# Kernel optimization log

Measured on AMD Instinct MI355X. Metric: run time of the kernel, lower is better.

The kernel has to match this reference:

```python
import jax, jax.numpy as jnp
import numpy as np
from jax import lax

D_MODEL, D_STATE, D_CONV, EXPAND = 192, 16, 3, 2
D_INNER = EXPAND * D_MODEL          # 384
DT_RANK = -(-D_MODEL // 16)         # 12
LN_EPS = 1e-5


def setup_inputs() -> dict:
    key = jax.random.key(0)
    ks = jax.random.split(key, 12)
    B, H, W = 4, 64, 64
    inv_sq = lambda n: 1.0 / np.sqrt(n)
    x = jax.random.normal(ks[0], (B, H, W, D_MODEL), jnp.float32)
    prompt = jax.random.normal(ks[1], (B, H, W, D_MODEL), jnp.float32)
    W_in = jax.random.normal(ks[2], (D_MODEL, 2 * D_INNER), jnp.float32) * inv_sq(D_MODEL)
    conv_w = jax.random.normal(ks[3], (D_INNER, 1, D_CONV, D_CONV), jnp.float32) * inv_sq(D_CONV * D_CONV)
    conv_b = jax.random.normal(ks[4], (D_INNER,), jnp.float32) * 0.02
    Wx = jax.random.normal(ks[5], (D_INNER, DT_RANK + 2 * D_STATE), jnp.float32) * inv_sq(D_INNER)
    Wdt = jax.random.uniform(ks[6], (DT_RANK, D_INNER), jnp.float32, -DT_RANK ** -0.5, DT_RANK ** -0.5)
    # dt bias init: inverse softplus of dt ~ LogUniform(1e-3, 0.1)
    dt = jnp.exp(jax.random.uniform(ks[7], (D_INNER,), jnp.float32) * (np.log(0.1) - np.log(1e-3)) + np.log(1e-3))
    dt = jnp.clip(dt, 1e-4, None)
    b_dt = dt + jnp.log(-jnp.expm1(-dt))
    A_log = jnp.log(jnp.broadcast_to(jnp.arange(1, D_STATE + 1, dtype=jnp.float32), (D_INNER, D_STATE)))
    D = jnp.ones((D_INNER,), jnp.float32)
    Wp = jax.random.normal(ks[8], (D_MODEL, D_STATE), jnp.float32) * inv_sq(D_MODEL)
    ln_g = jnp.ones((D_INNER,), jnp.float32)
    ln_b = jnp.zeros((D_INNER,), jnp.float32)
    Wout = jax.random.normal(ks[9], (D_INNER, D_MODEL), jnp.float32) * inv_sq(D_INNER)
    return dict(x=x, prompt=prompt, W_in=W_in, conv_w=conv_w, conv_b=conv_b, Wx=Wx,
                Wdt=Wdt, b_dt=b_dt, A_log=A_log, D=D, Wp=Wp, ln_g=ln_g, ln_b=ln_b, Wout=Wout)


def _selective_scan(u, delta, A, Bs, Cs, D):
    # u, delta: [B, L, d]; Bs, Cs: [B, L, n]; A: [d, n]; D: [d]
    Bsz = u.shape[0]
    h0 = jnp.zeros((Bsz, D_INNER, D_STATE), u.dtype)

    def step(h, inp):
        dl, uu, b, c = inp                      # [B,d],[B,d],[B,n],[B,n]
        dA = jnp.exp(dl[..., None] * A)          # [B,d,n]
        h = dA * h + (dl * uu)[..., None] * b[:, None, :]
        y = jnp.einsum('bdn,bn->bd', h, c)
        return h, y

    xs = (jnp.moveaxis(delta, 1, 0), jnp.moveaxis(u, 1, 0),
          jnp.moveaxis(Bs, 1, 0), jnp.moveaxis(Cs, 1, 0))
    _, ys = lax.scan(step, h0, xs)               # ys: [L,B,d]
    return jnp.moveaxis(ys, 0, 1) + u * D        # [B,L,d]


def reference(x, prompt, W_in, conv_w, conv_b, Wx, Wdt, b_dt, A_log, D, Wp, ln_g, ln_b, Wout):
    B, H, W, C = x.shape
    L = H * W
    xz = x @ W_in                                 # [B,H,W,2*d_inner]
    xi, z = jnp.split(xz, 2, axis=-1)
    # depthwise conv2d (NCHW, groups=d_inner)
    xc = jnp.transpose(xi, (0, 3, 1, 2))
    pad = (D_CONV - 1) // 2
    xc = lax.conv_general_dilated(xc, conv_w, (1, 1), [(pad, pad), (pad, pad)],
                                  dimension_numbers=('NCHW', 'OIHW', 'NCHW'),
                                  feature_group_count=D_INNER)
    xc = xc + conv_b[None, :, None, None]
    xc = jax.nn.silu(xc)
    u = jnp.transpose(xc.reshape(B, D_INNER, L), (0, 2, 1))   # [B,L,d]
    x_dbl = u @ Wx                                            # [B,L,r+2n]
    dtr = x_dbl[..., :DT_RANK]
    Bs = x_dbl[..., DT_RANK:DT_RANK + D_STATE]
    Cs = x_dbl[..., DT_RANK + D_STATE:]
    delta = jax.nn.softplus(dtr @ Wdt + b_dt)                 # [B,L,d] (delta_bias + softplus)
    Cs = Cs + prompt.reshape(B, L, C) @ Wp                    # prompt-conditioned C
    A = -jnp.exp(A_log)                                       # [d,n]
    y = _selective_scan(u, delta, A, Bs, Cs, D)               # [B,L,d]
    # out_norm (LayerNorm over d_inner)
    mu = jnp.mean(y, axis=-1, keepdims=True)
    var = jnp.mean(jnp.square(y - mu), axis=-1, keepdims=True)
    y = (y - mu) * lax.rsqrt(var + LN_EPS) * ln_g + ln_b
    y = y.reshape(B, H, W, D_INNER)
    y = y * jax.nn.silu(z)
    return y @ Wout
```

## Files before the change

### kernel.cpp

```cpp
#include <hip/hip_runtime.h>
#include <hip/hip_bf16.h>

#define BB 4
#define HH 64
#define WW 64
#define LL 4096
#define DM 192
#define DI 384
#define NS 16
#define RK 12
#define NC 256
#define CH 16
#define ROWS 16384
#define XDS 64
#define LOG2E 1.44269504f

typedef __bf16 bf16x8 __attribute__((ext_vector_type(8)));
typedef float  f32x4  __attribute__((ext_vector_type(4)));

#if defined(__has_builtin)
#if __has_builtin(__builtin_amdgcn_exp2f)
#define fexp2(x) __builtin_amdgcn_exp2f(x)
#else
#define fexp2(x) exp2f(x)
#endif
#else
#define fexp2(x) exp2f(x)
#endif

__device__ __forceinline__ float fsilu(float x) {
    return x / (1.0f + __expf(-x));
}

__device__ __forceinline__ unsigned short f2bf(float f) {
    unsigned int u = __float_as_uint(f);
    unsigned int r = (u + 0x7fffu + ((u >> 16) & 1u)) >> 16;
    return (unsigned short)r;
}

__global__ __launch_bounds__(256) void f32_to_bf16_vec(
    const float* __restrict__ src, unsigned short* __restrict__ dst, int n4)
{
    int i = blockIdx.x * 256 + threadIdx.x;
    if (i < n4) {
        float4 v = ((const float4*)src)[i];
        ((ushort4*)dst)[i] = make_ushort4(f2bf(v.x), f2bf(v.y), f2bf(v.z), f2bf(v.w));
    }
}

__global__ __launch_bounds__(256) void build_bt(
    const float* __restrict__ src, unsigned short* __restrict__ dst,
    int K, int Nsrc, int Nrows)
{
    int idx = blockIdx.x * 256 + threadIdx.x;
    if (idx >= Nrows * K) return;
    int n = idx / K, k = idx % K;
    dst[idx] = (n < Nsrc) ? f2bf(src[k * Nsrc + n]) : (unsigned short)0;
}

template<bool SPLIT>
__global__ __launch_bounds__(256) void gemm_bf16_mfma(
    const unsigned short* __restrict__ A, const unsigned short* __restrict__ BT,
    float* __restrict__ C0, float* __restrict__ C1,
    int M, int N, int K, int halfN)
{
    __shared__ __align__(16) char lds[64 * 80 * 2];
    char* As = lds;
    char* Bs = lds + 64 * 80;
    const int tid = threadIdx.x;
    const int w = tid >> 6, lane = tid & 63;
    const int wm = w >> 1, wn = w & 1;
    const int row0 = blockIdx.x * 64, col0 = blockIdx.y * 64;
    const int r = tid >> 2, cch = tid & 3;
    const int l15 = lane & 15, k8 = lane >> 4;

    f32x4 acc[2][2] = {};
    for (int k0 = 0; k0 < K; k0 += 32) {
        *(float4*)(As + r * 80 + cch * 16) =
            *(const float4*)(A + (size_t)(row0 + r) * K + k0 + cch * 8);
        *(float4*)(Bs + r * 80 + cch * 16) =
            *(const float4*)(BT + (size_t)(col0 + r) * K + k0 + cch * 8);
        __syncthreads();
        bf16x8 a0 = *(const bf16x8*)(As + (wm * 32 +      l15) * 80 + k8 * 16);
        bf16x8 a1 = *(const bf16x8*)(As + (wm * 32 + 16 + l15) * 80 + k8 * 16);
        bf16x8 b0 = *(const bf16x8*)(Bs + (wn * 32 +      l15) * 80 + k8 * 16);
        bf16x8 b1 = *(const bf16x8*)(Bs + (wn * 32 + 16 + l15) * 80 + k8 * 16);
        acc[0][0] = __builtin_amdgcn_mfma_f32_16x16x32_bf16(a0, b0, acc[0][0], 0, 0, 0);
        acc[0][1] = __builtin_amdgcn_mfma_f32_16x16x32_bf16(a0, b1, acc[0][1], 0, 0, 0);
        acc[1][0] = __builtin_amdgcn_mfma_f32_16x16x32_bf16(a1, b0, acc[1][0], 0, 0, 0);
        acc[1][1] = __builtin_amdgcn_mfma_f32_16x16x32_bf16(a1, b1, acc[1][1], 0, 0, 0);
        __syncthreads();
    }

    float* Cw;
    int cbase, cstride;
    if (SPLIT) {
        cstride = halfN;
        if (col0 < halfN) { Cw = C0; cbase = col0; }
        else              { Cw = C1; cbase = col0 - halfN; }
    } else {
        Cw = C0; cbase = col0; cstride = N;
    }
    #pragma unroll
    for (int fm = 0; fm < 2; ++fm)
        #pragma unroll
        for (int fn = 0; fn < 2; ++fn)
            #pragma unroll
            for (int reg = 0; reg < 4; ++reg) {
                int row = row0 + wm * 32 + fm * 16 + k8 * 4 + reg;
                int col = cbase + wn * 32 + fn * 16 + l15;
                Cw[(size_t)row * cstride + col] = acc[fm][fn][reg];
            }
}

__global__ __launch_bounds__(256) void conv_dw_silu(
    const float* __restrict__ xi, const float* __restrict__ conv_w,
    const float* __restrict__ conv_b, float* __restrict__ u,
    unsigned short* __restrict__ u_bf)
{
    int idx = blockIdx.x * 256 + threadIdx.x;
    int c4 = idx % 96;
    int rest = idx / 96;
    int w = rest % WW; rest /= WW;
    int h = rest % HH;
    int b = rest / HH;
    int c = c4 * 4;

    float wgt[4][9];
    #pragma unroll
    for (int q = 0; q < 4; ++q)
        #pragma unroll
        for (int t = 0; t < 9; ++t)
            wgt[q][t] = conv_w[(c + q) * 9 + t];

    float4 acc = *(const float4*)&conv_b[c];
    #pragma unroll
    for (int kh = 0; kh < 3; ++kh) {
        int hh = h + kh - 1;
        if ((unsigned)hh >= HH) continue;
        #pragma unroll
        for (int kw = 0; kw < 3; ++kw) {
            int ww = w + kw - 1;
            if ((unsigned)ww >= WW) continue;
            const float4 xv = *(const float4*)&xi[(((size_t)(b * HH + hh)) * WW + ww) * DI + c];
            int t = kh * 3 + kw;
            acc.x += xv.x * wgt[0][t];
            acc.y += xv.y * wgt[1][t];
            acc.z += xv.z * wgt[2][t];
            acc.w += xv.w * wgt[3][t];
        }
    }
    acc.x = fsilu(acc.x); acc.y = fsilu(acc.y);
    acc.z = fsilu(acc.z); acc.w = fsilu(acc.w);
    size_t off = (((size_t)b * LL) + h * WW + w) * DI + c;
    *(float4*)&u[off] = acc;
    *(ushort4*)&u_bf[off] = make_ushort4(f2bf(acc.x), f2bf(acc.y), f2bf(acc.z), f2bf(acc.w));
}

__global__ __launch_bounds__(256) void post_proj(
    const float* __restrict__ xdbl, const float* __restrict__ prompt,
    const float* __restrict__ Wdt, const float* __restrict__ b_dt,
    const float* __restrict__ Wp,
    float* __restrict__ delta, float* __restrict__ Csv)
{
    const int wid = threadIdx.x >> 6, lane = threadIdx.x & 63;
    const int row = blockIdx.x * 4 + wid;

    const float4* dp = (const float4*)&xdbl[(size_t)row * XDS];
    const float4 d0 = dp[0], d1 = dp[1], d2 = dp[2];
    const float dtr[RK] = {d0.x, d0.y, d0.z, d0.w, d1.x, d1.y, d1.z, d1.w,
                           d2.x, d2.y, d2.z, d2.w};

    const int n16 = lane & 15, g = lane >> 4;
    const float* prow = prompt + (size_t)row * DM + g * 48;
    float pw = 0.f;
    #pragma unroll
    for (int cc = 0; cc < 48; cc += 4) {
        const float4 p4 = *(const float4*)&prow[cc];
        const int c = g * 48 + cc;
        pw += p4.x * Wp[(c    ) * NS + n16];
        pw += p4.y * Wp[(c + 1) * NS + n16];
        pw += p4.z * Wp[(c + 2) * NS + n16];
        pw += p4.w * Wp[(c + 3) * NS + n16];
    }
    pw += __shfl_xor(pw, 16);
    pw += __shfl_xor(pw, 32);
    if (lane < 16)
        Csv[(size_t)row * NS + lane] = xdbl[(size_t)row * XDS + 28 + lane] + pw;

    #pragma unroll
    for (int jj = 0; jj < 6; ++jj) {
        int dch = jj * 64 + lane;
        float acc = b_dt[dch];
        #pragma unroll
        for (int r = 0; r < RK; ++r) acc += dtr[r] * Wdt[r * DI + dch];
        delta[(size_t)row * DI + dch] = (acc > 20.f) ? acc : log1pf(__expf(acc));
    }
}

__global__ __launch_bounds__(256) void scan_p1_v4(
    const float* __restrict__ delta, const float* __restrict__ u,
    const float* __restrict__ xdbl, const float* __restrict__ A_log,
    float* __restrict__ AH)
{
    const int g = blockIdx.x * 256 + threadIdx.x;
    const int d = g % DI;
    const int bc = g / DI;
    const int b = bc / NC, c = bc % NC;

    float Adn[NS], h[NS];
    {
        const float4* ap4 = (const float4*)(A_log + d * NS);
        #pragma unroll
        for (int q = 0; q < 4; ++q) {
            const float4 v = ap4[q];
            Adn[q*4+0] = -__expf(v.x) * LOG2E;
            Adn[q*4+1] = -__expf(v.y) * LOG2E;
            Adn[q*4+2] = -__expf(v.z) * LOG2E;
            Adn[q*4+3] = -__expf(v.w) * LOG2E;
        }
    }
    #pragma unroll
    for (int n = 0; n < NS; ++n) h[n] = 0.f;

    const size_t rbase = (size_t)(b * LL + c * CH);
    const float* dp = delta + rbase * DI + d;
    const float* up = u     + rbase * DI + d;
    const float* xp = xdbl  + rbase * XDS + 12;

    float dlt = dp[0], uu = up[0];
    float4 bb0 = *(const float4*)(xp + 0), bb1 = *(const float4*)(xp + 4);
    float4 bb2 = *(const float4*)(xp + 8), bb3 = *(const float4*)(xp + 12);
    float sdlt = 0.f;

    for (int i = 0; i < CH; ++i) {
        const float dlt_n = dp[(i + 1) * DI];
        const float uu_n  = up[(i + 1) * DI];
        const float* xn = xp + (i + 1) * XDS;
        const float4 bn0 = *(const float4*)(xn + 0), bn1 = *(const float4*)(xn + 4);
        const float4 bn2 = *(const float4*)(xn + 8), bn3 = *(const float4*)(xn + 12);

        const float du = dlt * uu;
        sdlt += dlt;
        const float bs[NS] = {bb0.x, bb0.y, bb0.z, bb0.w, bb1.x, bb1.y, bb1.z, bb1.w,
                              bb2.x, bb2.y, bb2.z, bb2.w, bb3.x, bb3.y, bb3.z, bb3.w};
        #pragma unroll
        for (int n = 0; n < NS; ++n) {
            const float a = fexp2(dlt * Adn[n]);
            h[n] = a * h[n] + du * bs[n];
        }
        dlt = dlt_n; uu = uu_n;
        bb0 = bn0; bb1 = bn1; bb2 = bn2; bb3 = bn3;
    }
    float* dst = AH + 2 * (((size_t)bc * DI + d) * NS);
    #pragma unroll
    for (int q = 0; q < 8; ++q) {
        const float ap0 = fexp2(sdlt * Adn[2*q]);
        const float ap1 = fexp2(sdlt * Adn[2*q+1]);
        *(float4*)(dst + 4 * q) = make_float4(ap0, h[2*q], ap1, h[2*q+1]);
    }
}

__global__ __launch_bounds__(256) void scan_p2(float2* __restrict__ AH)
{
    const int gid = blockIdx.x * 256 + threadIdx.x;
    const int dn = gid % (DI * NS);
    const int b  = gid / (DI * NS);
    const size_t base = (size_t)b * NC * DI * NS + dn;
    const size_t cs = (size_t)DI * NS;

    float2 buf[4];
    #pragma unroll
    for (int k = 0; k < 4; ++k) buf[k] = AH[base + (size_t)k * cs];

    float hin = 0.f;
    for (int c = 0; c < NC; c += 4) {
        #pragma unroll
        for (int k = 0; k < 4; ++k) {
            const int cn = (c + k + 4 < NC) ? (c + k + 4) : (NC - 1);
            const float2 nxt = AH[base + (size_t)cn * cs];
            const float2 cur = buf[k];
            AH[base + (size_t)(c + k) * cs].x = hin;
            hin = cur.x * hin + cur.y;
            buf[k] = nxt;
        }
    }
}

__global__ __launch_bounds__(384) void scan_p3_ln(
    const float* __restrict__ delta, const float* __restrict__ u,
    const float* __restrict__ xdbl, const float* __restrict__ Csv,
    const float* __restrict__ AH, const float* __restrict__ A_log,
    const float* __restrict__ Dvec, const float* __restrict__ z,
    const float* __restrict__ ln_g, const float* __restrict__ ln_b,
    unsigned short* __restrict__ yin_bf)
{
    __shared__ float red_s[2][8], red_sq[2][8];
    const int d = threadIdx.x;
    const int bc = blockIdx.x;
    const int b = bc / NC, c = bc % NC;
    const int wid = d >> 6, lane = d & 63;

    float Adn[NS], h[NS];
    {
        const float4* ap4 = (const float4*)(A_log + d * NS);
        #pragma unroll
        for (int q = 0; q < 4; ++q) {
            const float4 v = ap4[q];
            Adn[q*4+0] = -__expf(v.x) * LOG2E;
            Adn[q*4+1] = -__expf(v.y) * LOG2E;
            Adn[q*4+2] = -__expf(v.z) * LOG2E;
            Adn[q*4+3] = -__expf(v.w) * LOG2E;
        }
    }
    {
        const float* hp = AH + 2 * (((size_t)bc * DI + d) * NS);
        #pragma unroll
        for (int q = 0; q < 8; ++q) {
            const float4 v = *(const float4*)(hp + 4 * q);
            h[2*q] = v.x; h[2*q+1] = v.z;
        }
    }
    const float Dd = Dvec[d];
    const float lg = ln_g[d], lb = ln_b[d];

    const size_t rbase = (size_t)(b * LL + c * CH);
    const float* dp = delta + rbase * DI + d;
    const float* up = u     + rbase * DI + d;
    const float* zp = z     + rbase * DI + d;
    const float* xp = xdbl  + rbase * XDS + 12;
    const float* cp = Csv   + rbase * NS;
    unsigned short* yp = yin_bf + rbase * DI + d;

    float dlt = dp[0], uu = up[0], zz = zp[0];
    float4 bb0 = *(const float4*)(xp + 0), bb1 = *(const float4*)(xp + 4);
    float4 bb2 = *(const float4*)(xp + 8), bb3 = *(const float4*)(xp + 12);
    float4 cc0 = *(const float4*)(cp + 0), cc1 = *(const float4*)(cp + 4);
    float4 cc2 = *(const float4*)(cp + 8), cc3 = *(const float4*)(cp + 12);

    for (int i = 0; i < CH; ++i) {
        const float dlt_n = dp[(i + 1) * DI];
        const float uu_n  = up[(i + 1) * DI];
        const float zz_n  = zp[(i + 1) * DI];
        const float* xn = xp + (i + 1) * XDS;
        const float* cn = cp + (i + 1) * NS;
        const float4 bn0 = *(const float4*)(xn + 0), bn1 = *(const float4*)(xn + 4);
        const float4 bn2 = *(const float4*)(xn + 8), bn3 = *(const float4*)(xn + 12);
        const float4 cn0 = *(const float4*)(cn + 0), cn1 = *(const float4*)(cn + 4);
        const float4 cn2 = *(const float4*)(cn + 8), cn3 = *(const float4*)(cn + 12);

        const float du = dlt * uu;
        const float bs[NS] = {bb0.x, bb0.y, bb0.z, bb0.w, bb1.x, bb1.y, bb1.z, bb1.w,
                              bb2.x, bb2.y, bb2.z, bb2.w, bb3.x, bb3.y, bb3.z, bb3.w};
        const float cs[NS] = {cc0.x, cc0.y, cc0.z, cc0.w, cc1.x, cc1.y, cc1.z, cc1.w,
                              cc2.x, cc2.y, cc2.z, cc2.w, cc3.x, cc3.y, cc3.z, cc3.w};
        float acc = uu * Dd;
        #pragma unroll
        for (int n = 0; n < NS; ++n) {
            const float a = fexp2(dlt * Adn[n]);
            h[n] = a * h[n] + du * bs[n];
            acc += h[n] * cs[n];
        }
        float s = acc, sq = acc * acc;
        #pragma unroll
        for (int m = 1; m < 64; m <<= 1) {
            s  += __shfl_xor(s, m);
            sq += __shfl_xor(sq, m);
        }
        const int par = i & 1;
        if (lane == 0) { red_s[par][wid] = s; red_sq[par][wid] = sq; }
        __syncthreads();
        s = red_s[par][0] + red_s[par][1] + red_s[par][2]
          + red_s[par][3] + red_s[par][4] + red_s[par][5];
        sq = red_sq[par][0] + red_sq[par][1] + red_sq[par][2]
           + red_sq[par][3] + red_sq[par][4] + red_sq[par][5];
        const float mu = s * (1.f / DI);
        const float var = sq * (1.f / DI) - mu * mu;
        const float inv = rsqrtf(var + 1e-5f);
        const float yn = (acc - mu) * inv * lg + lb;
        yp[(size_t)i * DI] = f2bf(yn * fsilu(zz));

        dlt = dlt_n; uu = uu_n; zz = zz_n;
        bb0 = bn0; bb1 = bn1; bb2 = bn2; bb3 = bn3;
        cc0 = cn0; cc1 = cn1; cc2 = cn2; cc3 = cn3;
    }
}

extern "C" void kernel_launch(void* const* d_in, const int* in_sizes, int n_in,
                              void* d_out, int out_size, void* d_ws, size_t ws_size,
                              hipStream_t stream)
{
    const float* x      = (const float*)d_in[0];
    const float* prompt = (const float*)d_in[1];
    const float* W_in   = (const float*)d_in[2];
    const float* conv_w = (const float*)d_in[3];
    const float* conv_b = (const float*)d_in[4];
    const float* Wx     = (const float*)d_in[5];
    const float* Wdt    = (const float*)d_in[6];
    const float* b_dt   = (const float*)d_in[7];
    const float* A_log  = (const float*)d_in[8];
    const float* Dvec   = (const float*)d_in[9];
    const float* Wp     = (const float*)d_in[10];
    const float* ln_g   = (const float*)d_in[11];
    const float* ln_b   = (const float*)d_in[12];
    const float* Wout   = (const float*)d_in[13];
    float* out = (float*)d_out;

    char* ws = (char*)d_ws;
    const size_t SZ_BLD = (size_t)ROWS * DI * 4;
    float* xi    = (float*)(ws);
    float* z     = (float*)(ws + SZ_BLD);
    float* u     = (float*)(ws + 2 * SZ_BLD);
    float* delta = (float*)(ws + 3 * SZ_BLD);
    char*  p     = ws + 4 * SZ_BLD;
    float* xdbl  = (float*)p;            p += (size_t)ROWS * XDS * 4;
    float* Csv   = (float*)p;            p += (size_t)ROWS * NS * 4;
    char*  ahreg = p;
    float* AH    = (float*)p;            p += (size_t)BB * NC * DI * NS * 8;
    unsigned short* WinT   = (unsigned short*)p;  p += (size_t)(2 * DI) * DM * 2;
    unsigned short* WxPadT = (unsigned short*)p;  p += (size_t)XDS * DI * 2;
    unsigned short* WoutT  = (unsigned short*)p;  p += (size_t)DM * DI * 2;
    unsigned short* x_bf   = (unsigned short*)ahreg;
    unsigned short* u_bf   = (unsigned short*)(ahreg + (size_t)ROWS * DM * 2);
    unsigned short* yin_bf = (unsigned short*)xi;

    f32_to_bf16_vec<<<(ROWS * DM / 4 + 255) / 256, 256, 0, stream>>>(x, x_bf, ROWS * DM / 4);
    build_bt<<<(2 * DI * DM + 255) / 256, 256, 0, stream>>>(W_in, WinT, DM, 2 * DI, 2 * DI);
    build_bt<<<(XDS * DI + 255) / 256, 256, 0, stream>>>(Wx, WxPadT, DI, 44, XDS);
    build_bt<<<(DM * DI + 255) / 256, 256, 0, stream>>>(Wout, WoutT, DI, DM, DM);

    {
        dim3 g(ROWS / 64, (2 * DI) / 64);
        gemm_bf16_mfma<true><<<g, 256, 0, stream>>>(x_bf, WinT, xi, z, ROWS, 2 * DI, DM, DI);
    }
    conv_dw_silu<<<(BB * HH * WW * 96) / 256, 256, 0, stream>>>(xi, conv_w, conv_b, u, u_bf);
    {
        dim3 g(ROWS / 64, 1);
        gemm_bf16_mfma<false><<<g, 256, 0, stream>>>(u_bf, WxPadT, xdbl, nullptr, ROWS, XDS, DI, 0);
    }
    post_proj<<<ROWS / 4, 256, 0, stream>>>(xdbl, prompt, Wdt, b_dt, Wp, delta, Csv);
    scan_p1_v4<<<(BB * NC * DI) / 256, 256, 0, stream>>>(delta, u, xdbl, A_log, AH);
    scan_p2<<<(BB * DI * NS) / 256, 256, 0, stream>>>((float2*)AH);
    scan_p3_ln<<<BB * NC, 384, 0, stream>>>(delta, u, xdbl, Csv, AH, A_log,
                                            Dvec, z, ln_g, ln_b, yin_bf);
    {
        dim3 g(ROWS / 64, DM / 64);
        gemm_bf16_mfma<false><<<g, 256, 0, stream>>>(yin_bf, WoutT, out, nullptr, ROWS, DM, DI, 0);
    }
}
```

Measured before the change: 290.0 us.

## Fuse prompt projection into x_proj GEMM and recompute delta inside scan

Concatenates u and prompt along K into one bf16 operand so a single GEMM produces dt-rank, B and prompt-conditioned C, which removes the post_proj kernel and the separate Csv buffer. Delta is no longer stored; both scan passes recompute it from the 12 dt-rank values and Wdt per step. u and z are now kept only in bf16, which cuts scan memory traffic but adds per-step FMAs and transcendentals, and lowers the precision of u and z in the scan.

```diff
diff --git a/kernel.cpp b/kernel.cpp
--- a/kernel.cpp
+++ b/kernel.cpp
@@ -13,7 +13,9 @@
 #define CH 16
 #define ROWS 16384
 #define XDS 64
+#define KA 576
 #define LOG2E 1.44269504f
+#define LN2   0.69314718f
 
 typedef __bf16 bf16x8 __attribute__((ext_vector_type(8)));
 typedef float  f32x4  __attribute__((ext_vector_type(4)));
@@ -37,6 +39,9 @@
     unsigned int r = (u + 0x7fffu + ((u >> 16) & 1u)) >> 16;
     return (unsigned short)r;
 }
+__device__ __forceinline__ float bf2f(unsigned short v) {
+    return __uint_as_float((unsigned int)v << 16);
+}
 
 __global__ __launch_bounds__(256) void f32_to_bf16_vec(
     const float* __restrict__ src, unsigned short* __restrict__ dst, int n4)
@@ -48,6 +53,17 @@
     }
 }
 
+__global__ __launch_bounds__(256) void prompt_to_across(
+    const float* __restrict__ prompt, unsigned short* __restrict__ Across)
+{
+    int i4 = blockIdx.x * 256 + threadIdx.x;
+    if (i4 >= ROWS * (DM / 4)) return;
+    int row = i4 / (DM / 4), c4 = i4 % (DM / 4);
+    float4 v = ((const float4*)prompt)[i4];
+    *(ushort4*)&Across[(size_t)row * KA + DI + c4 * 4] =
+        make_ushort4(f2bf(v.x), f2bf(v.y), f2bf(v.z), f2bf(v.w));
+}
+
 __global__ __launch_bounds__(256) void build_bt(
     const float* __restrict__ src, unsigned short* __restrict__ dst,
     int K, int Nsrc, int Nrows)
@@ -58,10 +74,23 @@
     dst[idx] = (n < Nsrc) ? f2bf(src[k * Nsrc + n]) : (unsigned short)0;
 }
 
+__global__ __launch_bounds__(256) void build_bxt(
+    const float* __restrict__ Wx, const float* __restrict__ Wp,
+    unsigned short* __restrict__ dst)
+{
+    int idx = blockIdx.x * 256 + threadIdx.x;
+    if (idx >= XDS * KA) return;
+    int n = idx / KA, k = idx % KA;
+    float v = 0.f;
+    if (k < DI) { if (n < 44) v = Wx[k * 44 + n]; }
+    else        { if (n >= 28 && n < 44) v = Wp[(k - DI) * NS + (n - 28)]; }
+    dst[idx] = f2bf(v);
+}
+
 template<bool SPLIT>
 __global__ __launch_bounds__(256) void gemm_bf16_mfma(
     const unsigned short* __restrict__ A, const unsigned short* __restrict__ BT,
-    float* __restrict__ C0, float* __restrict__ C1,
+    float* __restrict__ C0, unsigned short* __restrict__ C1z,
     int M, int N, int K, int halfN)
 {
     __shared__ __align__(16) char lds[64 * 80 * 2];
@@ -92,31 +121,36 @@
         __syncthreads();
     }
 
-    float* Cw;
-    int cbase, cstride;
-    if (SPLIT) {
-        cstride = halfN;
-        if (col0 < halfN) { Cw = C0; cbase = col0; }
-        else              { Cw = C1; cbase = col0 - halfN; }
+    if (SPLIT && col0 >= halfN) {
+        const int cbase = col0 - halfN;
+        #pragma unroll
+        for (int fm = 0; fm < 2; ++fm)
+            #pragma unroll
+            for (int fn = 0; fn < 2; ++fn)
+                #pragma unroll
+                for (int reg = 0; reg < 4; ++reg) {
+                    int row = row0 + wm * 32 + fm * 16 + k8 * 4 + reg;
+                    int col = cbase + wn * 32 + fn * 16 + l15;
+                    C1z[(size_t)row * halfN + col] = f2bf(acc[fm][fn][reg]);
+                }
     } else {
-        Cw = C0; cbase = col0; cstride = N;
-    }
-    #pragma unroll
-    for (int fm = 0; fm < 2; ++fm)
-        #pragma unroll
-        for (int fn = 0; fn < 2; ++fn)
+        const int cstride = SPLIT ? halfN : N;
+        #pragma unroll
+        for (int fm = 0; fm < 2; ++fm)
             #pragma unroll
-            for (int reg = 0; reg < 4; ++reg) {
-                int row = row0 + wm * 32 + fm * 16 + k8 * 4 + reg;
-                int col = cbase + wn * 32 + fn * 16 + l15;
-                Cw[(size_t)row * cstride + col] = acc[fm][fn][reg];
-            }
+            for (int fn = 0; fn < 2; ++fn)
+                #pragma unroll
+                for (int reg = 0; reg < 4; ++reg) {
+                    int row = row0 + wm * 32 + fm * 16 + k8 * 4 + reg;
+                    int col = col0 + wn * 32 + fn * 16 + l15;
+                    C0[(size_t)row * cstride + col] = acc[fm][fn][reg];
+                }
+    }
 }
 
 __global__ __launch_bounds__(256) void conv_dw_silu(
     const float* __restrict__ xi, const float* __restrict__ conv_w,
-    const float* __restrict__ conv_b, float* __restrict__ u,
-    unsigned short* __restrict__ u_bf)
+    const float* __restrict__ conv_b, unsigned short* __restrict__ Across)
 {
     int idx = blockIdx.x * 256 + threadIdx.x;
     int c4 = idx % 96;
@@ -152,56 +186,14 @@
     }
     acc.x = fsilu(acc.x); acc.y = fsilu(acc.y);
     acc.z = fsilu(acc.z); acc.w = fsilu(acc.w);
-    size_t off = (((size_t)b * LL) + h * WW + w) * DI + c;
-    *(float4*)&u[off] = acc;
-    *(ushort4*)&u_bf[off] = make_ushort4(f2bf(acc.x), f2bf(acc.y), f2bf(acc.z), f2bf(acc.w));
-}
-
-__global__ __launch_bounds__(256) void post_proj(
-    const float* __restrict__ xdbl, const float* __restrict__ prompt,
-    const float* __restrict__ Wdt, const float* __restrict__ b_dt,
-    const float* __restrict__ Wp,
-    float* __restrict__ delta, float* __restrict__ Csv)
-{
-    const int wid = threadIdx.x >> 6, lane = threadIdx.x & 63;
-    const int row = blockIdx.x * 4 + wid;
-
-    const float4* dp = (const float4*)&xdbl[(size_t)row * XDS];
-    const float4 d0 = dp[0], d1 = dp[1], d2 = dp[2];
-    const float dtr[RK] = {d0.x, d0.y, d0.z, d0.w, d1.x, d1.y, d1.z, d1.w,
-                           d2.x, d2.y, d2.z, d2.w};
-
-    const int n16 = lane & 15, g = lane >> 4;
-    const float* prow = prompt + (size_t)row * DM + g * 48;
-    float pw = 0.f;
-    #pragma unroll
-    for (int cc = 0; cc < 48; cc += 4) {
-        const float4 p4 = *(const float4*)&prow[cc];
-        const int c = g * 48 + cc;
-        pw += p4.x * Wp[(c    ) * NS + n16];
-        pw += p4.y * Wp[(c + 1) * NS + n16];
-        pw += p4.z * Wp[(c + 2) * NS + n16];
-        pw += p4.w * Wp[(c + 3) * NS + n16];
-    }
-    pw += __shfl_xor(pw, 16);
-    pw += __shfl_xor(pw, 32);
-    if (lane < 16)
-        Csv[(size_t)row * NS + lane] = xdbl[(size_t)row * XDS + 28 + lane] + pw;
-
-    #pragma unroll
-    for (int jj = 0; jj < 6; ++jj) {
-        int dch = jj * 64 + lane;
-        float acc = b_dt[dch];
-        #pragma unroll
-        for (int r = 0; r < RK; ++r) acc += dtr[r] * Wdt[r * DI + dch];
-        delta[(size_t)row * DI + dch] = (acc > 20.f) ? acc : log1pf(__expf(acc));
-    }
-}
-
-__global__ __launch_bounds__(256) void scan_p1_v4(
-    const float* __restrict__ delta, const float* __restrict__ u,
-    const float* __restrict__ xdbl, const float* __restrict__ A_log,
-    float* __restrict__ AH)
+    size_t off = (((size_t)b * LL) + h * WW + w) * KA + c;
+    *(ushort4*)&Across[off] = make_ushort4(f2bf(acc.x), f2bf(acc.y), f2bf(acc.z), f2bf(acc.w));
+}
+
+__global__ __launch_bounds__(256) void scan_p1_v5(
+    const unsigned short* __restrict__ uA, const float* __restrict__ xdbl,
+    const float* __restrict__ A_log, const float* __restrict__ Wdt,
+    const float* __restrict__ b_dt, float* __restrict__ AH)
 {
     const int g = blockIdx.x * 256 + threadIdx.x;
     const int d = g % DI;
@@ -220,25 +212,37 @@
             Adn[q*4+3] = -__expf(v.w) * LOG2E;
         }
     }
+    float wdt[RK];
+    #pragma unroll
+    for (int r = 0; r < RK; ++r) wdt[r] = Wdt[r * DI + d];
+    const float bdt = b_dt[d];
     #pragma unroll
     for (int n = 0; n < NS; ++n) h[n] = 0.f;
 
     const size_t rbase = (size_t)(b * LL + c * CH);
-    const float* dp = delta + rbase * DI + d;
-    const float* up = u     + rbase * DI + d;
-    const float* xp = xdbl  + rbase * XDS + 12;
-
-    float dlt = dp[0], uu = up[0];
-    float4 bb0 = *(const float4*)(xp + 0), bb1 = *(const float4*)(xp + 4);
-    float4 bb2 = *(const float4*)(xp + 8), bb3 = *(const float4*)(xp + 12);
+    const unsigned short* up = uA + rbase * KA + d;
+    const float* xp = xdbl + rbase * XDS;
+
+    float uu = bf2f(up[0]);
+    float4 bb0 = *(const float4*)(xp + 12), bb1 = *(const float4*)(xp + 16);
+    float4 bb2 = *(const float4*)(xp + 20), bb3 = *(const float4*)(xp + 24);
     float sdlt = 0.f;
 
     for (int i = 0; i < CH; ++i) {
-        const float dlt_n = dp[(i + 1) * DI];
-        const float uu_n  = up[(i + 1) * DI];
-        const float* xn = xp + (i + 1) * XDS;
-        const float4 bn0 = *(const float4*)(xn + 0), bn1 = *(const float4*)(xn + 4);
-        const float4 bn2 = *(const float4*)(xn + 8), bn3 = *(const float4*)(xn + 12);
+        const float* xr = xp + (size_t)i * XDS;
+        const float4 t0 = *(const float4*)(xr + 0);
+        const float4 t1 = *(const float4*)(xr + 4);
+        const float4 t2 = *(const float4*)(xr + 8);
+        const float uu_n = bf2f(up[(size_t)(i + 1) * KA]);
+        const float* xn = xp + (size_t)(i + 1) * XDS;
+        const float4 bn0 = *(const float4*)(xn + 12), bn1 = *(const float4*)(xn + 16);
+        const float4 bn2 = *(const float4*)(xn + 20), bn3 = *(const float4*)(xn + 24);
+
+        float t = bdt;
+        t += t0.x * wdt[0] + t0.y * wdt[1] + t0.z * wdt[2]  + t0.w * wdt[3];
+        t += t1.x * wdt[4] + t1.y * wdt[5] + t1.z * wdt[6]  + t1.w * wdt[7];
+        t += t2.x * wdt[8] + t2.y * wdt[9] + t2.z * wdt[10] + t2.w * wdt[11];
+        const float dlt = (t > 20.f) ? t : LN2 * __log2f(1.f + fexp2(t * LOG2E));
 
         const float du = dlt * uu;
         sdlt += dlt;
@@ -249,7 +253,7 @@
             const float a = fexp2(dlt * Adn[n]);
             h[n] = a * h[n] + du * bs[n];
         }
-        dlt = dlt_n; uu = uu_n;
+        uu = uu_n;
         bb0 = bn0; bb1 = bn1; bb2 = bn2; bb3 = bn3;
     }
     float* dst = AH + 2 * (((size_t)bc * DI + d) * NS);
@@ -287,11 +291,11 @@
     }
 }
 
-__global__ __launch_bounds__(384) void scan_p3_ln(
-    const float* __restrict__ delta, const float* __restrict__ u,
-    const float* __restrict__ xdbl, const float* __restrict__ Csv,
-    const float* __restrict__ AH, const float* __restrict__ A_log,
-    const float* __restrict__ Dvec, const float* __restrict__ z,
+__global__ __launch_bounds__(384) void scan_p3_ln_v3(
+    const unsigned short* __restrict__ uA, const unsigned short* __restrict__ z_bf,
+    const float* __restrict__ xdbl, const float* __restrict__ AH,
+    const float* __restrict__ A_log, const float* __restrict__ Wdt,
+    const float* __restrict__ b_dt, const float* __restrict__ Dvec,
     const float* __restrict__ ln_g, const float* __restrict__ ln_b,
     unsigned short* __restrict__ yin_bf)
 {
@@ -313,6 +317,10 @@
             Adn[q*4+3] = -__expf(v.w) * LOG2E;
         }
     }
+    float wdt[RK];
+    #pragma unroll
+    for (int r = 0; r < RK; ++r) wdt[r] = Wdt[r * DI + d];
+    const float bdt = b_dt[d];
     {
         const float* hp = AH + 2 * (((size_t)bc * DI + d) * NS);
         #pragma unroll
@@ -325,29 +333,35 @@
     const float lg = ln_g[d], lb = ln_b[d];
 
     const size_t rbase = (size_t)(b * LL + c * CH);
-    const float* dp = delta + rbase * DI + d;
-    const float* up = u     + rbase * DI + d;
-    const float* zp = z     + rbase * DI + d;
-    const float* xp = xdbl  + rbase * XDS + 12;
-    const float* cp = Csv   + rbase * NS;
+    const unsigned short* up = uA + rbase * KA + d;
+    const unsigned short* zp = z_bf + rbase * DI + d;
+    const float* xp = xdbl + rbase * XDS;
     unsigned short* yp = yin_bf + rbase * DI + d;
 
-    float dlt = dp[0], uu = up[0], zz = zp[0];
-    float4 bb0 = *(const float4*)(xp + 0), bb1 = *(const float4*)(xp + 4);
-    float4 bb2 = *(const float4*)(xp + 8), bb3 = *(const float4*)(xp + 12);
-    float4 cc0 = *(const float4*)(cp + 0), cc1 = *(const float4*)(cp + 4);
-    float4 cc2 = *(const float4*)(cp + 8), cc3 = *(const float4*)(cp + 12);
+    float uu = bf2f(up[0]), zz = bf2f(zp[0]);
+    float4 bb0 = *(const float4*)(xp + 12), bb1 = *(const float4*)(xp + 16);
+    float4 bb2 = *(const float4*)(xp + 20), bb3 = *(const float4*)(xp + 24);
+    float4 cc0 = *(const float4*)(xp + 28), cc1 = *(const float4*)(xp + 32);
+    float4 cc2 = *(const float4*)(xp + 36), cc3 = *(const float4*)(xp + 40);
 
     for (int i = 0; i < CH; ++i) {
-        const float dlt_n = dp[(i + 1) * DI];
-        const float uu_n  = up[(i + 1) * DI];
-        const float zz_n  = zp[(i + 1) * DI];
-        const float* xn = xp + (i + 1) * XDS;
-        const float* cn = cp + (i + 1) * NS;
-        const float4 bn0 = *(const float4*)(xn + 0), bn1 = *(const float4*)(xn + 4);
-        const float4 bn2 = *(const float4*)(xn + 8), bn3 = *(const float4*)(xn + 12);
-        const float4 cn0 = *(const float4*)(cn + 0), cn1 = *(const float4*)(cn + 4);
-        const float4 cn2 = *(const float4*)(cn + 8), cn3 = *(const float4*)(cn + 12);
+        const float* xr = xp + (size_t)i * XDS;
+        const float4 t0 = *(const float4*)(xr + 0);
+        const float4 t1 = *(const float4*)(xr + 4);
+        const float4 t2 = *(const float4*)(xr + 8);
+        const float uu_n = bf2f(up[(size_t)(i + 1) * KA]);
+        const float zz_n = bf2f(zp[(size_t)(i + 1) * DI]);
+        const float* xn = xp + (size_t)(i + 1) * XDS;
+        const float4 bn0 = *(const float4*)(xn + 12), bn1 = *(const float4*)(xn + 16);
+        const float4 bn2 = *(const float4*)(xn + 20), bn3 = *(const float4*)(xn + 24);
+        const float4 cn0 = *(const float4*)(xn + 28), cn1 = *(const float4*)(xn + 32);
+        const float4 cn2 = *(const float4*)(xn + 36), cn3 = *(const float4*)(xn + 40);
+
+        float t = bdt;
+        t += t0.x * wdt[0] + t0.y * wdt[1] + t0.z * wdt[2]  + t0.w * wdt[3];
+        t += t1.x * wdt[4] + t1.y * wdt[5] + t1.z * wdt[6]  + t1.w * wdt[7];
+        t += t2.x * wdt[8] + t2.y * wdt[9] + t2.z * wdt[10] + t2.w * wdt[11];
+        const float dlt = (t > 20.f) ? t : LN2 * __log2f(1.f + fexp2(t * LOG2E));
 
         const float du = dlt * uu;
         const float bs[NS] = {bb0.x, bb0.y, bb0.z, bb0.w, bb1.x, bb1.y, bb1.z, bb1.w,
@@ -380,7 +394,7 @@
         const float yn = (acc - mu) * inv * lg + lb;
         yp[(size_t)i * DI] = f2bf(yn * fsilu(zz));
 
-        dlt = dlt_n; uu = uu_n; zz = zz_n;
+        uu = uu_n; zz = zz_n;
         bb0 = bn0; bb1 = bn1; bb2 = bn2; bb3 = bn3;
         cc0 = cn0; cc1 = cn1; cc2 = cn2; cc3 = cn3;
     }
@@ -406,43 +420,38 @@
     const float* Wout   = (const float*)d_in[13];
     float* out = (float*)d_out;
 
-    char* ws = (char*)d_ws;
-    const size_t SZ_BLD = (size_t)ROWS * DI * 4;
-    float* xi    = (float*)(ws);
-    float* z     = (float*)(ws + SZ_BLD);
-    float* u     = (float*)(ws + 2 * SZ_BLD);
-    float* delta = (float*)(ws + 3 * SZ_BLD);
-    char*  p     = ws + 4 * SZ_BLD;
-    float* xdbl  = (float*)p;            p += (size_t)ROWS * XDS * 4;
-    float* Csv   = (float*)p;            p += (size_t)ROWS * NS * 4;
-    char*  ahreg = p;
-    float* AH    = (float*)p;            p += (size_t)BB * NC * DI * NS * 8;
-    unsigned short* WinT   = (unsigned short*)p;  p += (size_t)(2 * DI) * DM * 2;
-    unsigned short* WxPadT = (unsigned short*)p;  p += (size_t)XDS * DI * 2;
-    unsigned short* WoutT  = (unsigned short*)p;  p += (size_t)DM * DI * 2;
-    unsigned short* x_bf   = (unsigned short*)ahreg;
-    unsigned short* u_bf   = (unsigned short*)(ahreg + (size_t)ROWS * DM * 2);
+    char* p = (char*)d_ws;
+    float* xi = (float*)p;                 p += (size_t)ROWS * DI * 4;
+    unsigned short* z_bf = (unsigned short*)p;  p += (size_t)(ROWS + 1) * DI * 2;
+    unsigned short* Across = (unsigned short*)p; p += (size_t)(ROWS + 1) * KA * 2;
+    float* xdbl = (float*)p;               p += (size_t)(ROWS + 1) * XDS * 4;
+    char* ahreg = p;
+    float* AH = (float*)p;                 p += (size_t)BB * NC * DI * NS * 8;
+    unsigned short* WinT  = (unsigned short*)p;  p += (size_t)(2 * DI) * DM * 2;
+    unsigned short* BxT   = (unsigned short*)p;  p += (size_t)XDS * KA * 2;
+    unsigned short* WoutT = (unsigned short*)p;  p += (size_t)DM * DI * 2;
+    unsigned short* x_bf = (unsigned short*)ahreg;
     unsigned short* yin_bf = (unsigned short*)xi;
 
     f32_to_bf16_vec<<<(ROWS * DM / 4 + 255) / 256, 256, 0, stream>>>(x, x_bf, ROWS * DM / 4);
+    prompt_to_across<<<(ROWS * (DM / 4) + 255) / 256, 256, 0, stream>>>(prompt, Across);
     build_bt<<<(2 * DI * DM + 255) / 256, 256, 0, stream>>>(W_in, WinT, DM, 2 * DI, 2 * DI);
-    build_bt<<<(XDS * DI + 255) / 256, 256, 0, stream>>>(Wx, WxPadT, DI, 44, XDS);
+    build_bxt<<<(XDS * KA + 255) / 256, 256, 0, stream>>>(Wx, Wp, BxT);
     build_bt<<<(DM * DI + 255) / 256, 256, 0, stream>>>(Wout, WoutT, DI, DM, DM);
 
     {
         dim3 g(ROWS / 64, (2 * DI) / 64);
-        gemm_bf16_mfma<true><<<g, 256, 0, stream>>>(x_bf, WinT, xi, z, ROWS, 2 * DI, DM, DI);
-    }
-    conv_dw_silu<<<(BB * HH * WW * 96) / 256, 256, 0, stream>>>(xi, conv_w, conv_b, u, u_bf);
+        gemm_bf16_mfma<true><<<g, 256, 0, stream>>>(x_bf, WinT, xi, z_bf, ROWS, 2 * DI, DM, DI);
+    }
+    conv_dw_silu<<<(BB * HH * WW * 96) / 256, 256, 0, stream>>>(xi, conv_w, conv_b, Across);
     {
         dim3 g(ROWS / 64, 1);
-        gemm_bf16_mfma<false><<<g, 256, 0, stream>>>(u_bf, WxPadT, xdbl, nullptr, ROWS, XDS, DI, 0);
-    }
-    post_proj<<<ROWS / 4, 256, 0, stream>>>(xdbl, prompt, Wdt, b_dt, Wp, delta, Csv);
-    scan_p1_v4<<<(BB * NC * DI) / 256, 256, 0, stream>>>(delta, u, xdbl, A_log, AH);
+        gemm_bf16_mfma<false><<<g, 256, 0, stream>>>(Across, BxT, xdbl, nullptr, ROWS, XDS, KA, 0);
+    }
+    scan_p1_v5<<<(BB * NC * DI) / 256, 256, 0, stream>>>(Across, xdbl, A_log, Wdt, b_dt, AH);
     scan_p2<<<(BB * DI * NS) / 256, 256, 0, stream>>>((float2*)AH);
-    scan_p3_ln<<<BB * NC, 384, 0, stream>>>(delta, u, xdbl, Csv, AH, A_log,
-                                            Dvec, z, ln_g, ln_b, yin_bf);
+    scan_p3_ln_v3<<<BB * NC, 384, 0, stream>>>(Across, z_bf, xdbl, AH, A_log, Wdt,
+                                               b_dt, Dvec, ln_g, ln_b, yin_bf);
     {
         dim3 g(ROWS / 64, DM / 64);
         gemm_bf16_mfma<false><<<g, 256, 0, stream>>>(yin_bf, WoutT, out, nullptr, ROWS, DM, DI, 0);
```

New measurement: 279.3 us. 1.04x faster.
